# Kernel tuning notes

Measured on AMD Instinct MI355X. Metric: run time of the kernel, lower is better.

Reference implementation:

```python
import jax, jax.numpy as jnp
import numpy as np

B, N, DIM = 4, 1024, 1024
H, DH = 16, 64
NUM_MEM = 4
TOPK = 64
QK_SCALE = 10.0  # qk_norm_scale


def l2norm(t, eps=1e-12):
    # qk_norm_groups == 1 -> normalize over full head dim
    return t / jnp.clip(jnp.linalg.norm(t, axis=-1, keepdims=True), eps)


def setup_inputs() -> dict:
    key = jax.random.key(0)
    ks = jax.random.split(key, 12)
    s = 0.02
    inp = {
        "x": jax.random.normal(ks[0], (B, N, DIM), dtype=jnp.float32),
        "Wq": jax.random.normal(ks[1], (DIM, H * DH), dtype=jnp.float32) * s,
        "Wk": jax.random.normal(ks[2], (DIM, H * DH), dtype=jnp.float32) * s,
        "Wv": jax.random.normal(ks[3], (DIM, H * DH), dtype=jnp.float32) * s,
        "W_pre_th": jax.random.normal(ks[4], (H, H), dtype=jnp.float32) * (1.0 / H) ** 0.5,
        "W_post_th": jax.random.normal(ks[5], (H, H), dtype=jnp.float32) * (1.0 / H) ** 0.5,
        "mem_k": jax.random.normal(ks[6], (H, NUM_MEM, DH), dtype=jnp.float32),
        "mem_v": jax.random.normal(ks[7], (H, NUM_MEM, DH), dtype=jnp.float32),
        "head_scale_params": jnp.ones((1, H, 1, 1), dtype=jnp.float32),
        "Wg": jax.random.normal(ks[8], (DIM, H * DH), dtype=jnp.float32) * s,
        "bg": jnp.ones((H * DH,), dtype=jnp.float32),
        "Wo": jax.random.normal(ks[9], (H * DH, DIM), dtype=jnp.float32) * s,
    }
    return inp


def reference(x, Wq, Wk, Wv, W_pre_th, W_post_th, mem_k, mem_v,
              head_scale_params, Wg, bg, Wo):
    b, n, _ = x.shape
    # projections -> b h n d
    q = (x @ Wq).reshape(b, n, H, DH).transpose(0, 2, 1, 3)
    k = (x @ Wk).reshape(b, n, H, DH).transpose(0, 2, 1, 3)
    v = (x @ Wv).reshape(b, n, H, DH).transpose(0, 2, 1, 3)

    # memory key/values prepended along the key axis
    mk = jnp.broadcast_to(mem_k[None], (b, H, NUM_MEM, DH))
    mv = jnp.broadcast_to(mem_v[None], (b, H, NUM_MEM, DH))
    k = jnp.concatenate([mk, k], axis=2)
    v = jnp.concatenate([mv, v], axis=2)

    # qk-norm: l2 normalize then fixed scale
    q = l2norm(q)
    k = l2norm(k)

    dots = jnp.einsum("bhid,bhjd->bhij", q, k) * QK_SCALE  # b h n (n+m)
    # pre-softmax talking heads (1x1 conv over head channels)
    dots = jnp.einsum("hg,bgij->bhij", W_pre_th, dots)

    mask_value = -jnp.finfo(dots.dtype).max
    j = n + NUM_MEM
    # causal mask, left-padded False over the memory columns
    col_pos = jnp.arange(j) - NUM_MEM  # mem cols get negative pos -> never masked
    causal = jnp.arange(n)[:, None] < col_pos[None, :]  # (n, j)
    dots = jnp.where(causal[None, None], mask_value, dots)

    # sparse top-k: keep only entries >= k-th largest per row
    top = jax.lax.top_k(dots, TOPK)[0]
    vk = top[..., -1:]
    dots = jnp.where(dots < vk, mask_value, dots)

    attn = jax.nn.softmax(dots, axis=-1)
    # post-softmax talking heads
    attn = jnp.einsum("hg,bgij->bhij", W_post_th, attn)

    out = jnp.einsum("bhij,bhjd->bhid", attn, v)
    out = out * head_scale_params
    out = out.transpose(0, 2, 1, 3).reshape(b, n, H * DH)

    gates = x @ Wg + bg
    out = out * jax.nn.sigmoid(gates)
    return out @ Wo
```

## Files before the change

kernel.cpp:

```cpp
#include <hip/hip_runtime.h>
#include <hip/hip_bf16.h>
#include <float.h>

#define B_ 4
#define N_ 1024
#define H_ 16
#define DH_ 64
#define NM_ 4
#define J_ 1028
#define IT_ 4
#define JST 1064
#define TOPK_ 64
#define QKSCALE 10.0f
#define KTF_BG 67584
#define VTF_DC 16896

typedef __attribute__((ext_vector_type(8))) short short8;
typedef __attribute__((ext_vector_type(4))) float f32x4;
typedef __attribute__((ext_vector_type(8))) unsigned short ushort8;
typedef __attribute__((ext_vector_type(4))) unsigned int u32x4;
typedef __attribute__((ext_vector_type(2))) unsigned int u32x2;
typedef _Float16 half8 __attribute__((ext_vector_type(8)));

__device__ __forceinline__ unsigned short f2b(float f){
  union { float f; unsigned int i; } c; c.f = f;
  unsigned int r = c.i + 0x7FFFu + ((c.i >> 16) & 1u);
  return (unsigned short)(r >> 16);
}
__device__ __forceinline__ unsigned short f2h(float f){
  return __builtin_bit_cast(unsigned short, (_Float16)f);
}
__device__ __forceinline__ float h2f(unsigned short u){
  return (float)__builtin_bit_cast(_Float16, u);
}
__device__ __forceinline__ unsigned int h2key(unsigned int u){
  return (u & 0x8000u) ? (~u & 0xFFFFu) : (u | 0x8000u);
}
__device__ __forceinline__ float key2f(unsigned int k){
  unsigned int u = (k & 0x8000u) ? (k & 0x7FFFu) : (~k & 0xFFFFu);
  return h2f((unsigned short)u);
}

__global__ void k_cvtAll(const float* __restrict__ x,  const float* __restrict__ wq,
                         const float* __restrict__ wk, const float* __restrict__ wv,
                         const float* __restrict__ wg, const float* __restrict__ wo,
                         unsigned short* __restrict__ xb, unsigned short* __restrict__ wcat,
                         unsigned short* __restrict__ wob){
  const int NX = 4096 * 1024, NW = 1024 * 1024;
  int i = blockIdx.x * 256 + threadIdx.x;
  int st = gridDim.x * 256;
  for (; i < NX + 5 * NW; i += st){
    if (i < NX){ xb[i] = f2b(x[i]); }
    else {
      int k = i - NX;
      int which = k >> 20, off = k & (NW - 1);
      if (which == 4){ wob[off] = f2b(wo[off]); }
      else {
        const float* s = which == 0 ? wq : which == 1 ? wk : which == 2 ? wv : wg;
        wcat[(size_t)(off >> 10) * 4096 + which * 1024 + (off & 1023)] = f2b(s[off]);
      }
    }
  }
}

__global__ __launch_bounds__(256) void k_mem(const float* __restrict__ mk, const float* __restrict__ mv,
                                             unsigned short* __restrict__ ktF, unsigned short* __restrict__ vtF){
  int h = blockIdx.x * 4 + (threadIdx.x >> 6);
  int d = threadIdx.x & 63;
  unsigned short kh[4], vh[4];
  #pragma unroll
  for (int mm = 0; mm < 4; ++mm){
    float kv = mk[(h * 4 + mm) * 64 + d];
    float ss = kv * kv;
    #pragma unroll
    for (int off = 32; off; off >>= 1) ss += __shfl_xor(ss, off);
    kh[mm] = f2h(kv / fmaxf(sqrtf(ss), 1e-12f));
    vh[mm] = f2h(mv[(h * 4 + mm) * 64 + d]);
  }
  for (int b = 0; b < B_; ++b){
    int bg = b * 16 + h;
    #pragma unroll
    for (int mm = 0; mm < 4; ++mm)
      ktF[(size_t)bg * KTF_BG + (size_t)(d >> 5) * 512 + (mm + ((d >> 3) & 3) * 16) * 8 + (d & 7)] = kh[mm];
    #pragma unroll
    for (int mm = 0; mm < 4; ++mm)
      vtF[(size_t)bg * KTF_BG + (size_t)(d >> 4) * VTF_DC + (d & 15) * 8 + mm] = vh[mm];
    {
      unsigned int* kz = (unsigned int*)(ktF + (size_t)bg * KTF_BG + 64 * 1024);
      for (int c = d; c < 1024; c += 64) kz[c] = 0u;
    }
    #pragma unroll
    for (int dc = 0; dc < 4; ++dc){
      unsigned int* vz = (unsigned int*)(vtF + (size_t)bg * KTF_BG + (size_t)dc * VTF_DC + 32 * 512);
      for (int c = d; c < 256; c += 64) vz[c] = 0u;
    }
  }
}

__global__ __launch_bounds__(256) void k_gemmF(const unsigned short* __restrict__ A,
                                               const unsigned short* __restrict__ Wc,
                                               unsigned short* __restrict__ qn,
                                               unsigned short* __restrict__ ktF,
                                               unsigned short* __restrict__ vtF,
                                               unsigned short* __restrict__ gate,
                                               const float* __restrict__ bgv)
{
  __shared__ unsigned short As[128][40];
  __shared__ unsigned short Bs[64][40];
  const int t = threadIdx.x;
  const int m0 = blockIdx.y * 128, n0 = blockIdx.x * 64;
  const int l = t & 63, w = t >> 6;
  const int l15 = l & 15, l4 = l >> 4;

  f32x4 acc[2][4];
  #pragma unroll
  for (int a = 0; a < 2; ++a)
    #pragma unroll
    for (int b2 = 0; b2 < 4; ++b2) acc[a][b2] = (f32x4){0.f, 0.f, 0.f, 0.f};

  for (int k0 = 0; k0 < 1024; k0 += 32){
    #pragma unroll
    for (int cc = 0; cc < 2; ++cc){
      int c = t + cc * 256;
      int row = c >> 2, colc = (c & 3) * 8;
      *(ushort8*)&As[row][colc] = *(const ushort8*)&A[(m0 + row) * 1024 + k0 + colc];
    }
    {
      int kk = t >> 3, nc = (t & 7) * 8;
      ushort8 vb = *(const ushort8*)&Wc[(size_t)(k0 + kk) * 4096 + n0 + nc];
      #pragma unroll
      for (int e = 0; e < 8; ++e) Bs[nc + e][kk] = vb[e];
    }
    __syncthreads();
    short8 af[2], bfr[4];
    #pragma unroll
    for (int mf = 0; mf < 2; ++mf) af[mf]  = *(const short8*)&As[w * 32 + mf * 16 + l15][l4 * 8];
    #pragma unroll
    for (int nf = 0; nf < 4; ++nf) bfr[nf] = *(const short8*)&Bs[nf * 16 + l15][l4 * 8];
    #pragma unroll
    for (int mf = 0; mf < 2; ++mf)
      #pragma unroll
      for (int nf = 0; nf < 4; ++nf)
        acc[mf][nf] = __builtin_amdgcn_mfma_f32_16x16x32_bf16(af[mf], bfr[nf], acc[mf][nf], 0, 0, 0);
    __syncthreads();
  }

  const int which = n0 >> 10;
  const int ncol0 = n0 & 1023;
  const int hcol = ncol0 >> 6;
  #pragma unroll
  for (int mf = 0; mf < 2; ++mf){
    if (which == 2){
      int row0 = m0 + w * 32 + mf * 16 + l4 * 4;
      int bb = row0 >> 10;
      int j0 = (row0 & 1023) + NM_;
      int jtE = j0 >> 5, lj = (j0 & 31) >> 3, e0 = j0 & 7;
      #pragma unroll
      for (int nf = 0; nf < 4; ++nf){
        int col = ncol0 + nf * 16 + l15;
        int h = col >> 6, d = col & 63;
        unsigned int lo = (unsigned int)f2h(acc[mf][nf][0]) | ((unsigned int)f2h(acc[mf][nf][1]) << 16);
        unsigned int hi = (unsigned int)f2h(acc[mf][nf][2]) | ((unsigned int)f2h(acc[mf][nf][3]) << 16);
        unsigned short* dst = vtF + (size_t)(bb * 16 + h) * KTF_BG +
                              (size_t)(d >> 4) * VTF_DC + (size_t)jtE * 512 +
                              ((d & 15) + lj * 16) * 8 + e0;
        *(u32x2*)dst = (u32x2){lo, hi};
      }
    } else {
      #pragma unroll
      for (int r = 0; r < 4; ++r){
        int row = m0 + w * 32 + mf * 16 + l4 * 4 + r;
        float rn = 1.f;
        if (which <= 1){
          float ss = 0.f;
          #pragma unroll
          for (int nf = 0; nf < 4; ++nf) ss += acc[mf][nf][r] * acc[mf][nf][r];
          #pragma unroll
          for (int off = 1; off < 16; off <<= 1) ss += __shfl_xor(ss, off);
          rn = 1.f / fmaxf(sqrtf(ss), 1e-12f);
          if (which == 0) rn *= QKSCALE;
        }
        #pragma unroll
        for (int nf = 0; nf < 4; ++nf){
          int col = ncol0 + nf * 16 + l15;
          float v = acc[mf][nf][r];
          int bb = row >> 10, ii = row & 1023;
          if (which == 3){
            float g = v + bgv[3 * 1024 + col];
            gate[(size_t)row * 1024 + col] = f2h(1.f / (1.f + __expf(-g)));
          } else if (which == 0){
            int d = col & 63;
            qn[((size_t)(bb * H_ + hcol) * N_ + ii) * DH_ + d] = f2h(v * rn);
          } else {
            int j = ii + NM_;
            int d = col & 63;
            ktF[(size_t)(bb * 16 + hcol) * KTF_BG + (size_t)(j >> 4) * 1024 +
                (size_t)(d >> 5) * 512 + ((j & 15) + ((d >> 3) & 3) * 16) * 8 + (d & 7)]
              = f2h(v * rn);
          }
        }
      }
    }
  }
}

__global__ __launch_bounds__(256) void k_gemmO(const unsigned short* __restrict__ A,
                                               const unsigned short* __restrict__ W,
                                               float* __restrict__ outp)
{
  __shared__ unsigned short As[128][40];
  __shared__ unsigned short Bs[64][40];
  const int t = threadIdx.x;
  const int m0 = blockIdx.y * 128, n0 = blockIdx.x * 64;
  const int l = t & 63, w = t >> 6;
  const int l15 = l & 15, l4 = l >> 4;

  f32x4 acc[2][4];
  #pragma unroll
  for (int a = 0; a < 2; ++a)
    #pragma unroll
    for (int b2 = 0; b2 < 4; ++b2) acc[a][b2] = (f32x4){0.f, 0.f, 0.f, 0.f};

  for (int k0 = 0; k0 < 1024; k0 += 32){
    #pragma unroll
    for (int cc = 0; cc < 2; ++cc){
      int c = t + cc * 256;
      int row = c >> 2, colc = (c & 3) * 8;
      *(ushort8*)&As[row][colc] = *(const ushort8*)&A[(m0 + row) * 1024 + k0 + colc];
    }
    {
      int kk = t >> 3, nc = (t & 7) * 8;
      ushort8 vb = *(const ushort8*)&W[(k0 + kk) * 1024 + n0 + nc];
      #pragma unroll
      for (int e = 0; e < 8; ++e) Bs[nc + e][kk] = vb[e];
    }
    __syncthreads();
    short8 af[2], bfr[4];
    #pragma unroll
    for (int mf = 0; mf < 2; ++mf) af[mf]  = *(const short8*)&As[w * 32 + mf * 16 + l15][l4 * 8];
    #pragma unroll
    for (int nf = 0; nf < 4; ++nf) bfr[nf] = *(const short8*)&Bs[nf * 16 + l15][l4 * 8];
    #pragma unroll
    for (int mf = 0; mf < 2; ++mf)
      #pragma unroll
      for (int nf = 0; nf < 4; ++nf)
        acc[mf][nf] = __builtin_amdgcn_mfma_f32_16x16x32_bf16(af[mf], bfr[nf], acc[mf][nf], 0, 0, 0);
    __syncthreads();
  }

  #pragma unroll
  for (int mf = 0; mf < 2; ++mf)
    #pragma unroll
    for (int r = 0; r < 4; ++r){
      int row = m0 + w * 32 + mf * 16 + l4 * 4 + r;
      #pragma unroll
      for (int nf = 0; nf < 4; ++nf)
        outp[(size_t)row * 1024 + n0 + nf * 16 + l15] = acc[mf][nf][r];
    }
}

__global__ __launch_bounds__(1024) void k_attnM(
  const unsigned short* __restrict__ qn, const unsigned short* __restrict__ ktF,
  const unsigned short* __restrict__ vtF, const float* __restrict__ wpre,
  const float* __restrict__ wpost, const float* __restrict__ hsc,
  const unsigned short* __restrict__ gate, unsigned short* __restrict__ aout)
{
  __shared__ unsigned short sd[16 * IT_ * JST];
  __shared__ unsigned short qls[16 * 4 * 64];
  __shared__ unsigned short wpre16[16 * 32];
  __shared__ unsigned short wpost16[16 * 32];

  const int blk = blockIdx.x;
  const int b = (blk >> 1) & 3;
  const int idx = ((blk >> 3) << 1) | (blk & 1);
  const int it = 255 - idx;
  const int i0 = it * IT_;
  const int nAmax = i0 + IT_ + 4;
  const int nJtA = (nAmax + 15) >> 4;
  const int nJtE = (nAmax + 31) >> 5;
  const int nJtD = nJtE * 2;
  const int jc = nJtE * 32;
  const int t = threadIdx.x;
  const int w = t >> 6, l = t & 63;
  const int l15 = l & 15, l4 = l >> 4;

  if (t < 256){
    int h = t >> 4, g = t & 15;
    wpre16[h * 32 + g]       = f2h(wpre[h * 16 + g]);
    wpre16[h * 32 + 16 + g]  = 0;
    wpost16[h * 32 + g]      = f2h(wpost[h * 16 + g]);
    wpost16[h * 32 + 16 + g] = 0;
  }
  for (int c = t; c < 2048; c += 1024){
    int d2 = c & 31, ii = (c >> 5) & 3, g = c >> 7;
    ((unsigned int*)qls)[c] =
      *(const unsigned int*)(qn + ((size_t)(b * 16 + g) * N_ + i0 + ii) * 64 + d2 * 2);
  }
  __syncthreads();

  {
    const int nw16 = (nJtA > w) ? ((nJtA - w + 15) >> 4) : 0;
    const int ntask = nw16 * 16;
    if (ntask > 0){
      const int tmax = ntask - 1;
      const unsigned short* kl = ktF + (size_t)(b * 16) * KTF_BG + (size_t)l * 8;
      auto kp = [&](int task)->const unsigned short*{
        int tt = task > tmax ? tmax : task;
        int g = tt & 15, jti = tt >> 4;
        return kl + (size_t)g * KTF_BG + (((size_t)(w + jti * 16)) << 10);
      };
      const unsigned short* p0 = kp(0);
      const unsigned short* p1 = kp(1);
      half8 kA0 = *(const half8*)p0, kA1 = *(const half8*)(p0 + 512);
      half8 kB0 = *(const half8*)p1, kB1 = *(const half8*)(p1 + 512);
      for (int task = 0; task < ntask; task += 2){
        half8 cA0 = kA0, cA1 = kA1, cB0 = kB0, cB1 = kB1;
        const unsigned short* pa = kp(task + 2);
        const unsigned short* pb = kp(task + 3);
        kA0 = *(const half8*)pa; kA1 = *(const half8*)(pa + 512);
        kB0 = *(const half8*)pb; kB1 = *(const half8*)(pb + 512);
        #pragma unroll
        for (int s = 0; s < 2; ++s){
          const int tt = task + s;
          const int g = tt & 15, jt = w + ((tt >> 4) << 4);
          const unsigned short* qp = &qls[(g * 4 + (l15 & 3)) * 64 + l4 * 8];
          half8 qf0 = *(const half8*)(qp);
          half8 qf1 = *(const half8*)(qp + 32);
          f32x4 acc = (f32x4){0.f, 0.f, 0.f, 0.f};
          acc = __builtin_amdgcn_mfma_f32_16x16x32_f16(s ? cB0 : cA0, qf0, acc, 0, 0, 0);
          acc = __builtin_amdgcn_mfma_f32_16x16x32_f16(s ? cB1 : cA1, qf1, acc, 0, 0, 0);
          if (l15 < IT_){
            unsigned int pk0 = (unsigned int)f2h(acc[0]) | ((unsigned int)f2h(acc[1]) << 16);
            unsigned int pk1 = (unsigned int)f2h(acc[2]) | ((unsigned int)f2h(acc[3]) << 16);
            unsigned int* dst = (unsigned int*)&sd[(g * IT_ + l15) * JST + jt * 16 + l4 * 4];
            dst[0] = pk0; dst[1] = pk1;
          }
        }
      }
    }
  }
  __syncthreads();

  {
    half8 wa = *(const half8*)&wpre16[l15 * 32 + l4 * 8];
    const int ntask = IT_ * nJtA;
    for (int task = w; task < ntask; task += 16){
      const int ii = task & (IT_ - 1), jt = task >> 2;
      unsigned int fb[4] = {0u, 0u, 0u, 0u};
      if (l4 < 2){
        const unsigned short* src = &sd[((l4 * 8) * IT_ + ii) * JST + jt * 16 + l15];
        #pragma unroll
        for (int e = 0; e < 8; e += 2){
          unsigned int lo = src[(size_t)(e)     * IT_ * JST];
          unsigned int hi = src[(size_t)(e + 1) * IT_ * JST];
          fb[e >> 1] = (lo & 0xFFFFu) | (hi << 16);
        }
      }
      f32x4 acc = (f32x4){0.f, 0.f, 0.f, 0.f};
      acc = __builtin_amdgcn_mfma_f32_16x16x32_f16(wa, __builtin_bit_cast(half8, *(u32x4*)fb), acc, 0, 0, 0);
      #pragma unroll
      for (int r = 0; r < 4; ++r)
        sd[((l4 * 4 + r) * IT_ + ii) * JST + jt * 16 + l15] = f2h(acc[r]);
    }
  }
  __syncthreads();

  for (int rr = 0; rr < 4; ++rr){
    const int row = w * 4 + rr;
    const int g = row >> 2, ii = row & 3;
    const int nA = i0 + ii + 5;
    unsigned short* rowp = &sd[(g * IT_ + ii) * JST];
    unsigned int kw[9];
    #pragma unroll
    for (int grp = 0; grp < 9; ++grp){
      kw[grp] = 0u;
      if (grp * 128 < jc){
        int j = grp * 128 + l * 2;
        unsigned int u = (j < JST) ? *(const unsigned int*)(rowp + j) : 0u;
        unsigned int klo = h2key(u & 0xFFFFu);
        unsigned int khi = h2key(u >> 16);
        if (j     >= nA) klo = 0u;
        if (j + 1 >= nA) khi = 0u;
        kw[grp] = klo | (khi << 16);
      }
    }
    unsigned int kmx = 0u;
    #pragma unroll
    for (int grp = 0; grp < 9; ++grp){
      if (grp * 128 < jc){
        unsigned int m2 = max(kw[grp] >> 16, kw[grp] & 0xFFFFu);
        kmx = max(kmx, m2);
      }
    }
    #pragma unroll
    for (int off = 32; off; off >>= 1) kmx = max(kmx, (unsigned int)__shfl_xor((int)kmx, off));
    const float mx = key2f(kmx);

    unsigned int T = 0u;
    if (nA > TOPK_){
      for (int bit = 15; bit >= 2; --bit){
        unsigned int Tc = T | (1u << bit);
        int c = 0;
        #pragma unroll
        for (int grp = 0; grp < 9; ++grp){
          if (grp * 128 < jc){
            c += __popcll(__ballot((kw[grp] & 0xFFFFu) >= Tc));
            c += __popcll(__ballot((kw[grp] >> 16) >= Tc));
          }
        }
        if (c >= TOPK_){
          T = Tc;
          if (c == TOPK_) break;
        }
      }
    }
    if (T == 0u) T = 1u;

    float s = 0.f;
    float ev[18];
    #pragma unroll
    for (int grp = 0; grp < 9; ++grp){
      if (grp * 128 < jc){
        unsigned int klo = kw[grp] & 0xFFFFu, khi = kw[grp] >> 16;
        float elo = (klo >= T) ? __expf(key2f(klo) - mx) : 0.f;
        float ehi = (khi >= T) ? __expf(key2f(khi) - mx) : 0.f;
        ev[grp * 2] = elo; ev[grp * 2 + 1] = ehi;
        s += elo + ehi;
      }
    }
    #pragma unroll
    for (int off = 32; off; off >>= 1) s += __shfl_xor(s, off);
    float inv = 1.f / s;
    #pragma unroll
    for (int grp = 0; grp < 9; ++grp){
      if (grp * 128 < jc){
        int j = grp * 128 + l * 2;
        if (j < JST)
          *(unsigned int*)(rowp + j) =
            (unsigned int)f2h(ev[grp * 2] * inv) | ((unsigned int)f2h(ev[grp * 2 + 1] * inv) << 16);
      }
    }
  }
  __syncthreads();

  {
    const int ntask = IT_ * nJtD;
    for (int task = w; task < ntask; task += 16){
      const int ii = task & (IT_ - 1), jt = task >> 2;
      half8 wa = *(const half8*)&wpost16[l15 * 32 + l4 * 8];
      unsigned int fb[4] = {0u, 0u, 0u, 0u};
      if (l4 < 2){
        const unsigned short* src = &sd[((l4 * 8) * IT_ + ii) * JST + jt * 16 + l15];
        #pragma unroll
        for (int e = 0; e < 8; e += 2){
          unsigned int lo = src[(size_t)(e)     * IT_ * JST];
          unsigned int hi = src[(size_t)(e + 1) * IT_ * JST];
          fb[e >> 1] = (lo & 0xFFFFu) | (hi << 16);
        }
      }
      f32x4 acc = (f32x4){0.f, 0.f, 0.f, 0.f};
      acc = __builtin_amdgcn_mfma_f32_16x16x32_f16(wa, __builtin_bit_cast(half8, *(u32x4*)fb), acc, 0, 0, 0);
      #pragma unroll
      for (int r = 0; r < 4; ++r)
        sd[((l4 * 4 + r) * IT_ + ii) * JST + jt * 16 + l15] = f2h(acc[r]);
    }
  }
  __syncthreads();

  for (int task = w; task < 64; task += 16){
    const int h = task >> 2, dc = task & 3;
    const int bg = b * 16 + h;
    const unsigned short* vbase = vtF + (size_t)bg * KTF_BG + (size_t)dc * VTF_DC + (size_t)l * 8;
    const unsigned short* arow = &sd[(h * IT_ + (l15 & 3)) * JST + l4 * 8];
    const int jm = nJtE - 1;
    auto vp_ = [&](int jt)->const half8*{
      int tt = jt > jm ? jm : jt;
      return (const half8*)(vbase + ((size_t)tt << 9));
    };
    half8 vA = *vp_(0), vB = *vp_(1);
    f32x4 acc = (f32x4){0.f, 0.f, 0.f, 0.f};
    int jt = 0;
    for (; jt + 2 <= nJtE; jt += 2){
      half8 cA = vA, cB = vB;
      vA = *vp_(jt + 2); vB = *vp_(jt + 3);
      half8 af0 = *(const half8*)(arow + jt * 32);
      half8 af1 = *(const half8*)(arow + jt * 32 + 32);
      acc = __builtin_amdgcn_mfma_f32_16x16x32_f16(af0, cA, acc, 0, 0, 0);
      acc = __builtin_amdgcn_mfma_f32_16x16x32_f16(af1, cB, acc, 0, 0, 0);
    }
    if (jt < nJtE){
      half8 af0 = *(const half8*)(arow + jt * 32);
      acc = __builtin_amdgcn_mfma_f32_16x16x32_f16(af0, vA, acc, 0, 0, 0);
    }
    if (l4 == 0){
      const float hs = hsc[h];
      #pragma unroll
      for (int r = 0; r < IT_; ++r){
        const int irow = (b << 10) | (i0 + r);
        const size_t o = (size_t)irow * 1024 + h * 64 + dc * 16 + l15;
        aout[o] = f2b(acc[r] * hs * h2f(gate[o]));
      }
    }
  }
}

extern "C" void kernel_launch(void* const* d_in, const int* in_sizes, int n_in,
                              void* d_out, int out_size, void* d_ws, size_t ws_size,
                              hipStream_t stream) {
  const float* x     = (const float*)d_in[0];
  const float* Wq    = (const float*)d_in[1];
  const float* Wk    = (const float*)d_in[2];
  const float* Wv    = (const float*)d_in[3];
  const float* Wpre  = (const float*)d_in[4];
  const float* Wpost = (const float*)d_in[5];
  const float* mk    = (const float*)d_in[6];
  const float* mv    = (const float*)d_in[7];
  const float* hsc   = (const float*)d_in[8];
  const float* Wg    = (const float*)d_in[9];
  const float* bg    = (const float*)d_in[10];
  const float* Wo    = (const float*)d_in[11];
  float* out = (float*)d_out;

  char* ws = (char*)d_ws;
  size_t off = 0;
  auto alloc = [&](size_t bytes) -> void* {
    void* p = ws + off; off += (bytes + 255) & ~(size_t)255; return p;
  };
  unsigned short* xb   = (unsigned short*)alloc((size_t)4096 * 1024 * 2);
  unsigned short* wcat = (unsigned short*)alloc((size_t)1024 * 4096 * 2);
  unsigned short* wob  = (unsigned short*)alloc((size_t)1024 * 1024 * 2);
  unsigned short* qn   = (unsigned short*)alloc((size_t)B_ * H_ * N_ * DH_ * 2);
  unsigned short* ktF  = (unsigned short*)alloc((size_t)B_ * H_ * KTF_BG * 2);
  unsigned short* vtF  = (unsigned short*)alloc((size_t)B_ * H_ * KTF_BG * 2);
  unsigned short* gate = (unsigned short*)alloc((size_t)4096 * 1024 * 2);
  unsigned short* aout = (unsigned short*)alloc((size_t)4096 * 1024 * 2);

  k_cvtAll<<<2048, 256, 0, stream>>>(x, Wq, Wk, Wv, Wg, Wo, xb, wcat, wob);

  k_mem<<<4, 256, 0, stream>>>(mk, mv, ktF, vtF);

  k_gemmF<<<dim3(64, 32), 256, 0, stream>>>(xb, wcat, qn, ktF, vtF, gate, bg - 3 * 1024);

  k_attnM<<<1024, 1024, 0, stream>>>(qn, ktF, vtF, Wpre, Wpost, hsc, gate, aout);

  k_gemmO<<<dim3(16, 32), 256, 0, stream>>>(aout, wob, out);
}
```

Before: 368.4 us.

## Merge memory-KV setup into convert kernel, deepen GEMM K tile, reorder attention blocks

The tiny k_mem launch is folded into the conversion kernel as four extra blocks, removing one kernel launch. Both bf16 GEMMs now stage a K-tile of 64 instead of 32 per shared-memory round, halving the number of barrier pairs per block at the cost of more LDS. The causal attention blocks are now assigned rows in a serpentine order (heavy, light, heavy, light) rather than strictly heaviest first, to balance per-CU work across scheduling waves.

```diff
diff --git a/kernel.cpp b/kernel.cpp
--- a/kernel.cpp
+++ b/kernel.cpp
@@ -45,10 +45,45 @@
                          const float* __restrict__ wk, const float* __restrict__ wv,
                          const float* __restrict__ wg, const float* __restrict__ wo,
                          unsigned short* __restrict__ xb, unsigned short* __restrict__ wcat,
-                         unsigned short* __restrict__ wob){
+                         unsigned short* __restrict__ wob,
+                         const float* __restrict__ mk, const float* __restrict__ mv,
+                         unsigned short* __restrict__ ktF, unsigned short* __restrict__ vtF){
   const int NX = 4096 * 1024, NW = 1024 * 1024;
+  if (blockIdx.x >= 2044){
+    int h = (blockIdx.x - 2044) * 4 + (threadIdx.x >> 6);
+    int d = threadIdx.x & 63;
+    unsigned short kh[4], vh[4];
+    #pragma unroll
+    for (int mm = 0; mm < 4; ++mm){
+      float kv = mk[(h * 4 + mm) * 64 + d];
+      float ss = kv * kv;
+      #pragma unroll
+      for (int off = 32; off; off >>= 1) ss += __shfl_xor(ss, off);
+      kh[mm] = f2h(kv / fmaxf(sqrtf(ss), 1e-12f));
+      vh[mm] = f2h(mv[(h * 4 + mm) * 64 + d]);
+    }
+    for (int b = 0; b < B_; ++b){
+      int bg = b * 16 + h;
+      #pragma unroll
+      for (int mm = 0; mm < 4; ++mm)
+        ktF[(size_t)bg * KTF_BG + (size_t)(d >> 5) * 512 + (mm + ((d >> 3) & 3) * 16) * 8 + (d & 7)] = kh[mm];
+      #pragma unroll
+      for (int mm = 0; mm < 4; ++mm)
+        vtF[(size_t)bg * KTF_BG + (size_t)(d >> 4) * VTF_DC + (d & 15) * 8 + mm] = vh[mm];
+      {
+        unsigned int* kz = (unsigned int*)(ktF + (size_t)bg * KTF_BG + 64 * 1024);
+        for (int c = d; c < 1024; c += 64) kz[c] = 0u;
+      }
+      #pragma unroll
+      for (int dc = 0; dc < 4; ++dc){
+        unsigned int* vz = (unsigned int*)(vtF + (size_t)bg * KTF_BG + (size_t)dc * VTF_DC + 32 * 512);
+        for (int c = d; c < 256; c += 64) vz[c] = 0u;
+      }
+    }
+    return;
+  }
   int i = blockIdx.x * 256 + threadIdx.x;
-  int st = gridDim.x * 256;
+  const int st = 2044 * 256;
   for (; i < NX + 5 * NW; i += st){
     if (i < NX){ xb[i] = f2b(x[i]); }
     else {
@@ -63,40 +98,6 @@
   }
 }
 
-__global__ __launch_bounds__(256) void k_mem(const float* __restrict__ mk, const float* __restrict__ mv,
-                                             unsigned short* __restrict__ ktF, unsigned short* __restrict__ vtF){
-  int h = blockIdx.x * 4 + (threadIdx.x >> 6);
-  int d = threadIdx.x & 63;
-  unsigned short kh[4], vh[4];
-  #pragma unroll
-  for (int mm = 0; mm < 4; ++mm){
-    float kv = mk[(h * 4 + mm) * 64 + d];
-    float ss = kv * kv;
-    #pragma unroll
-    for (int off = 32; off; off >>= 1) ss += __shfl_xor(ss, off);
-    kh[mm] = f2h(kv / fmaxf(sqrtf(ss), 1e-12f));
-    vh[mm] = f2h(mv[(h * 4 + mm) * 64 + d]);
-  }
-  for (int b = 0; b < B_; ++b){
-    int bg = b * 16 + h;
-    #pragma unroll
-    for (int mm = 0; mm < 4; ++mm)
-      ktF[(size_t)bg * KTF_BG + (size_t)(d >> 5) * 512 + (mm + ((d >> 3) & 3) * 16) * 8 + (d & 7)] = kh[mm];
-    #pragma unroll
-    for (int mm = 0; mm < 4; ++mm)
-      vtF[(size_t)bg * KTF_BG + (size_t)(d >> 4) * VTF_DC + (d & 15) * 8 + mm] = vh[mm];
-    {
-      unsigned int* kz = (unsigned int*)(ktF + (size_t)bg * KTF_BG + 64 * 1024);
-      for (int c = d; c < 1024; c += 64) kz[c] = 0u;
-    }
-    #pragma unroll
-    for (int dc = 0; dc < 4; ++dc){
-      unsigned int* vz = (unsigned int*)(vtF + (size_t)bg * KTF_BG + (size_t)dc * VTF_DC + 32 * 512);
-      for (int c = d; c < 256; c += 64) vz[c] = 0u;
-    }
-  }
-}
-
 __global__ __launch_bounds__(256) void k_gemmF(const unsigned short* __restrict__ A,
                                                const unsigned short* __restrict__ Wc,
                                                unsigned short* __restrict__ qn,
@@ -105,8 +106,8 @@
                                                unsigned short* __restrict__ gate,
                                                const float* __restrict__ bgv)
 {
-  __shared__ unsigned short As[128][40];
-  __shared__ unsigned short Bs[64][40];
+  __shared__ unsigned short As[128][72];
+  __shared__ unsigned short Bs[64][72];
   const int t = threadIdx.x;
   const int m0 = blockIdx.y * 128, n0 = blockIdx.x * 64;
   const int l = t & 63, w = t >> 6;
@@ -118,30 +119,35 @@
     #pragma unroll
     for (int b2 = 0; b2 < 4; ++b2) acc[a][b2] = (f32x4){0.f, 0.f, 0.f, 0.f};
 
-  for (int k0 = 0; k0 < 1024; k0 += 32){
+  for (int k0 = 0; k0 < 1024; k0 += 64){
+    #pragma unroll
+    for (int cc = 0; cc < 4; ++cc){
+      int c = t + cc * 256;
+      int row = c >> 3, colc = (c & 7) * 8;
+      *(ushort8*)&As[row][colc] = *(const ushort8*)&A[(m0 + row) * 1024 + k0 + colc];
+    }
     #pragma unroll
     for (int cc = 0; cc < 2; ++cc){
       int c = t + cc * 256;
-      int row = c >> 2, colc = (c & 3) * 8;
-      *(ushort8*)&As[row][colc] = *(const ushort8*)&A[(m0 + row) * 1024 + k0 + colc];
-    }
-    {
-      int kk = t >> 3, nc = (t & 7) * 8;
+      int kk = c >> 3, nc = (c & 7) * 8;
       ushort8 vb = *(const ushort8*)&Wc[(size_t)(k0 + kk) * 4096 + n0 + nc];
       #pragma unroll
       for (int e = 0; e < 8; ++e) Bs[nc + e][kk] = vb[e];
     }
     __syncthreads();
-    short8 af[2], bfr[4];
-    #pragma unroll
-    for (int mf = 0; mf < 2; ++mf) af[mf]  = *(const short8*)&As[w * 32 + mf * 16 + l15][l4 * 8];
-    #pragma unroll
-    for (int nf = 0; nf < 4; ++nf) bfr[nf] = *(const short8*)&Bs[nf * 16 + l15][l4 * 8];
-    #pragma unroll
-    for (int mf = 0; mf < 2; ++mf)
-      #pragma unroll
-      for (int nf = 0; nf < 4; ++nf)
-        acc[mf][nf] = __builtin_amdgcn_mfma_f32_16x16x32_bf16(af[mf], bfr[nf], acc[mf][nf], 0, 0, 0);
+    #pragma unroll
+    for (int ks = 0; ks < 64; ks += 32){
+      short8 af[2], bfr[4];
+      #pragma unroll
+      for (int mf = 0; mf < 2; ++mf) af[mf]  = *(const short8*)&As[w * 32 + mf * 16 + l15][ks + l4 * 8];
+      #pragma unroll
+      for (int nf = 0; nf < 4; ++nf) bfr[nf] = *(const short8*)&Bs[nf * 16 + l15][ks + l4 * 8];
+      #pragma unroll
+      for (int mf = 0; mf < 2; ++mf)
+        #pragma unroll
+        for (int nf = 0; nf < 4; ++nf)
+          acc[mf][nf] = __builtin_amdgcn_mfma_f32_16x16x32_bf16(af[mf], bfr[nf], acc[mf][nf], 0, 0, 0);
+    }
     __syncthreads();
   }
 
@@ -208,8 +214,8 @@
                                                const unsigned short* __restrict__ W,
                                                float* __restrict__ outp)
 {
-  __shared__ unsigned short As[128][40];
-  __shared__ unsigned short Bs[64][40];
+  __shared__ unsigned short As[128][72];
+  __shared__ unsigned short Bs[64][72];
   const int t = threadIdx.x;
   const int m0 = blockIdx.y * 128, n0 = blockIdx.x * 64;
   const int l = t & 63, w = t >> 6;
@@ -221,30 +227,35 @@
     #pragma unroll
     for (int b2 = 0; b2 < 4; ++b2) acc[a][b2] = (f32x4){0.f, 0.f, 0.f, 0.f};
 
-  for (int k0 = 0; k0 < 1024; k0 += 32){
+  for (int k0 = 0; k0 < 1024; k0 += 64){
+    #pragma unroll
+    for (int cc = 0; cc < 4; ++cc){
+      int c = t + cc * 256;
+      int row = c >> 3, colc = (c & 7) * 8;
+      *(ushort8*)&As[row][colc] = *(const ushort8*)&A[(m0 + row) * 1024 + k0 + colc];
+    }
     #pragma unroll
     for (int cc = 0; cc < 2; ++cc){
       int c = t + cc * 256;
-      int row = c >> 2, colc = (c & 3) * 8;
-      *(ushort8*)&As[row][colc] = *(const ushort8*)&A[(m0 + row) * 1024 + k0 + colc];
-    }
-    {
-      int kk = t >> 3, nc = (t & 7) * 8;
-      ushort8 vb = *(const ushort8*)&W[(k0 + kk) * 1024 + n0 + nc];
+      int kk = c >> 3, nc = (c & 7) * 8;
+      ushort8 vb = *(const ushort8*)&W[(size_t)(k0 + kk) * 1024 + n0 + nc];
       #pragma unroll
       for (int e = 0; e < 8; ++e) Bs[nc + e][kk] = vb[e];
     }
     __syncthreads();
-    short8 af[2], bfr[4];
-    #pragma unroll
-    for (int mf = 0; mf < 2; ++mf) af[mf]  = *(const short8*)&As[w * 32 + mf * 16 + l15][l4 * 8];
-    #pragma unroll
-    for (int nf = 0; nf < 4; ++nf) bfr[nf] = *(const short8*)&Bs[nf * 16 + l15][l4 * 8];
-    #pragma unroll
-    for (int mf = 0; mf < 2; ++mf)
-      #pragma unroll
-      for (int nf = 0; nf < 4; ++nf)
-        acc[mf][nf] = __builtin_amdgcn_mfma_f32_16x16x32_bf16(af[mf], bfr[nf], acc[mf][nf], 0, 0, 0);
+    #pragma unroll
+    for (int ks = 0; ks < 64; ks += 32){
+      short8 af[2], bfr[4];
+      #pragma unroll
+      for (int mf = 0; mf < 2; ++mf) af[mf]  = *(const short8*)&As[w * 32 + mf * 16 + l15][ks + l4 * 8];
+      #pragma unroll
+      for (int nf = 0; nf < 4; ++nf) bfr[nf] = *(const short8*)&Bs[nf * 16 + l15][ks + l4 * 8];
+      #pragma unroll
+      for (int mf = 0; mf < 2; ++mf)
+        #pragma unroll
+        for (int nf = 0; nf < 4; ++nf)
+          acc[mf][nf] = __builtin_amdgcn_mfma_f32_16x16x32_bf16(af[mf], bfr[nf], acc[mf][nf], 0, 0, 0);
+    }
     __syncthreads();
   }
 
@@ -273,7 +284,8 @@
   const int blk = blockIdx.x;
   const int b = (blk >> 1) & 3;
   const int idx = ((blk >> 3) << 1) | (blk & 1);
-  const int it = 255 - idx;
+  const int rd = idx >> 6, jj = idx & 63;
+  const int it = (rd == 0) ? (255 - jj) : (rd == 1) ? (128 + jj) : (rd == 2) ? (127 - jj) : jj;
   const int i0 = it * IT_;
   const int nAmax = i0 + IT_ + 4;
   const int nJtA = (nAmax + 15) >> 4;
@@ -535,9 +547,8 @@
   unsigned short* gate = (unsigned short*)alloc((size_t)4096 * 1024 * 2);
   unsigned short* aout = (unsigned short*)alloc((size_t)4096 * 1024 * 2);
 
-  k_cvtAll<<<2048, 256, 0, stream>>>(x, Wq, Wk, Wv, Wg, Wo, xb, wcat, wob);
-
-  k_mem<<<4, 256, 0, stream>>>(mk, mv, ktF, vtF);
+  k_cvtAll<<<2048, 256, 0, stream>>>(x, Wq, Wk, Wv, Wg, Wo, xb, wcat, wob,
+                                     mk, mv, ktF, vtF);
 
   k_gemmF<<<dim3(64, 32), 256, 0, stream>>>(xb, wcat, qn, ktF, vtF, gate, bg - 3 * 1024);
 
```

Result: faster. 360.2 us (-2.2%).
